# Performance work log

Measured on AMD Instinct MI355X. Metric: run time of the kernel, lower is better.

Reference implementation:

```python
import jax, jax.numpy as jnp
import numpy as np

D_MODEL = 1024
H = 16
D_K = D_MODEL // H
B = 4
S = 2048


def setup_inputs() -> dict:
    key = jax.random.key(0)
    ks = jax.random.split(key, 7)
    q = jax.random.normal(ks[0], (B, S, D_MODEL), dtype=jnp.float32)
    k = jax.random.normal(ks[1], (B, S, D_MODEL), dtype=jnp.float32)
    v = jax.random.normal(ks[2], (B, S, D_MODEL), dtype=jnp.float32)
    # nn.Linear weights have shape (out_features, in_features); y = x @ W.T
    scale = 1.0 / np.sqrt(D_MODEL)
    w_q = jax.random.normal(ks[3], (D_MODEL, D_MODEL), dtype=jnp.float32) * scale
    w_k = jax.random.normal(ks[4], (D_MODEL, D_MODEL), dtype=jnp.float32) * scale
    w_v = jax.random.normal(ks[5], (D_MODEL, D_MODEL), dtype=jnp.float32) * scale
    w_o = jax.random.normal(ks[6], (D_MODEL, D_MODEL), dtype=jnp.float32) * scale
    mask = jnp.ones((1, 1, S, S), dtype=bool)  # broadcasts over [B,H,S,S]
    return {"q": q, "k": k, "v": v, "w_q": w_q, "w_k": w_k, "w_v": w_v,
            "w_o": w_o, "mask": mask}


def reference(q, k, v, w_q, w_k, w_v, w_o, mask):
    # projections (nn.Linear, no bias): x @ W.T
    query = jnp.einsum('bsd,ed->bse', q, w_q)
    key_p = jnp.einsum('bsd,ed->bse', k, w_k)
    value = jnp.einsum('bsd,ed->bse', v, w_v)
    # split heads: [B,S,D] -> [B,H,S,d_k]
    query = query.reshape(B, S, H, D_K).transpose(0, 2, 1, 3)
    key_p = key_p.reshape(B, S, H, D_K).transpose(0, 2, 1, 3)
    value = value.reshape(B, S, H, D_K).transpose(0, 2, 1, 3)
    # scaled dot-product attention (explicit softmax, as in source)
    scores = jnp.einsum('bhqd,bhkd->bhqk', query, key_p) / jnp.sqrt(
        jnp.asarray(D_K, dtype=query.dtype))
    scores = jnp.where(mask, scores, jnp.asarray(-1e9, dtype=scores.dtype))
    weights = jax.nn.softmax(scores, axis=-1)
    ctx = jnp.einsum('bhqk,bhkd->bhqd', weights, value)
    # merge heads and output projection
    ctx = ctx.transpose(0, 2, 1, 3).reshape(B, S, D_MODEL)
    return jnp.einsum('bsd,ed->bse', ctx, w_o)
```

## Files before the change

### kernel.cpp

```cpp
#include <hip/hip_runtime.h>
#include <hip/hip_bf16.h>
#include <stdint.h>
#include <math.h>

#define DM 1024
#define SS 2048
#define HH 16

typedef unsigned short u16;
typedef __attribute__((ext_vector_type(8))) short short8;
typedef __attribute__((ext_vector_type(4))) float f32x4;
typedef __attribute__((ext_vector_type(4))) unsigned short u16x4;

#define C_SCALE 0.18033688011112042f

__device__ __forceinline__ u16 f2bf(float f) {
    union { float f; uint32_t u; } v; v.f = f;
    uint32_t r = v.u + 0x7FFFu + ((v.u >> 16) & 1u);
    return (u16)(r >> 16);
}

__device__ __forceinline__ void async_cp16(const void* g, void* l) {
    __builtin_amdgcn_global_load_lds(
        reinterpret_cast<const __attribute__((address_space(1))) unsigned int*>(
            reinterpret_cast<uintptr_t>(g)),
        reinterpret_cast<__attribute__((address_space(3))) unsigned int*>(
            reinterpret_cast<uintptr_t>(l)),
        16, 0, 0);
}

__device__ __forceinline__ short8 pack8(const float4 a, const float4 b) {
    union { short8 s; struct { __hip_bfloat162 p0, p1, p2, p3; } p; } u;
    u.p.p0 = __float22bfloat162_rn(make_float2(a.x, a.y));
    u.p.p1 = __float22bfloat162_rn(make_float2(a.z, a.w));
    u.p.p2 = __float22bfloat162_rn(make_float2(b.x, b.y));
    u.p.p3 = __float22bfloat162_rn(make_float2(b.z, b.w));
    return u.s;
}

__global__ __launch_bounds__(256) void cast_w4(const float* __restrict__ w0,
                                               const float* __restrict__ w1,
                                               const float* __restrict__ w2,
                                               const float* __restrict__ w3,
                                               u16* __restrict__ o0,
                                               u16* __restrict__ o1,
                                               u16* __restrict__ o2,
                                               u16* __restrict__ o3)
{
    const uint32_t which = blockIdx.x >> 10;
    const uint32_t i = (blockIdx.x & 1023u) * 256u + threadIdx.x;
    const float* in = which == 0 ? w0 : which == 1 ? w1 : which == 2 ? w2 : w3;
    u16* out = which == 0 ? o0 : which == 1 ? o1 : which == 2 ? o2 : o3;
    float4 v = ((const float4*)in)[i];
    u16x4 p = { f2bf(v.x), f2bf(v.y), f2bf(v.z), f2bf(v.w) };
    ((u16x4*)out)[i] = p;
}

__global__ __launch_bounds__(256) void gemm_proj(const float* __restrict__ Aq,
                                                 const float* __restrict__ Ak,
                                                 const float* __restrict__ Av,
                                                 const u16* __restrict__ Bq,
                                                 const u16* __restrict__ Bk,
                                                 const u16* __restrict__ Bv,
                                                 u16* __restrict__ Cq,
                                                 u16* __restrict__ Ck,
                                                 u16* __restrict__ Cv)
{
    __shared__ char sm[32768];
    const uint32_t t = threadIdx.x;
    const uint32_t l = t & 63u, w = t >> 6;
    const uint32_t sw = (blockIdx.x & 7u) * 192u + (blockIdx.x >> 3);
    const uint32_t which = sw >> 9;
    const uint32_t inner = sw & 511u;
    const uint32_t bm = inner >> 3, bn = inner & 7u;
    const uint32_t wr = w >> 1, wc = w & 1u;

    const float* A = which == 0 ? Aq : which == 1 ? Ak : Av;
    const u16*   B = which == 0 ? Bq : which == 1 ? Bk : Bv;

    const uint32_t q15 = l & 15u, G = l >> 4, xq = q15 & 7u;
    const uint32_t vbg0 = q15 * 128u + ((G ^ (xq & 3u)) << 4) + ((xq >> 2) << 6);
    const uint32_t vA0 = wr * 8192u + vbg0,          vA1 = vA0 ^ 64u;
    const uint32_t vB0 = 16384u + wc * 8192u + vbg0, vB1 = vB0 ^ 64u;

    const float* aP[4];
    uint32_t aD[4];
    #pragma unroll
    for (uint32_t i = 0; i < 4; ++i) {
        const uint32_t j = i * 256u + t, row = j >> 3, cc = j & 7u;
        aP[i] = A + (size_t)(bm * 128u + row) * DM + cc * 8u;
        aD[i] = row * 128u + ((cc ^ (row & 7u)) << 4);
    }
    uint32_t La[4];
    const u16* bP[4];
    #pragma unroll
    for (uint32_t i = 0; i < 4; ++i) {
        La[i] = (i * 256u + t) * 16u;
        const uint32_t r = La[i] >> 7;
        const uint32_t c8 = ((La[i] >> 4) & 7u) ^ (r & 7u);
        bP[i] = B + (size_t)(bn * 128u + r) * DM + c8 * 8u;
    }

    f32x4 acc[4][4] = {};
    float4 av[4][2];
    #pragma unroll
    for (uint32_t i = 0; i < 4; ++i) {
        av[i][0] = *(const float4*)(aP[i]);
        av[i][1] = *(const float4*)(aP[i] + 4);
    }

    for (uint32_t k0 = 0; k0 < 1024; k0 += 64) {
        __syncthreads();
        #pragma unroll
        for (uint32_t i = 0; i < 4; ++i)
            *(short8*)(sm + aD[i]) = pack8(av[i][0], av[i][1]);
        #pragma unroll
        for (uint32_t i = 0; i < 4; ++i) async_cp16(bP[i] + k0, sm + 16384 + La[i]);
        __syncthreads();

        if (k0 != 960u) {
            #pragma unroll
            for (uint32_t i = 0; i < 4; ++i) {
                av[i][0] = *(const float4*)(aP[i] + k0 + 64u);
                av[i][1] = *(const float4*)(aP[i] + k0 + 68u);
            }
        }

        #pragma unroll
        for (uint32_t kk = 0; kk < 2; ++kk) {
            const uint32_t va = kk ? vA1 : vA0;
            const uint32_t vb = kk ? vB1 : vB0;
            short8 a[4], b[4];
            #pragma unroll
            for (uint32_t m = 0; m < 4; ++m)
                a[m] = *(const short8*)(sm + va + m * 2048u);
            #pragma unroll
            for (uint32_t n = 0; n < 4; ++n)
                b[n] = *(const short8*)(sm + vb + n * 2048u);
            #pragma unroll
            for (uint32_t m = 0; m < 4; ++m)
                #pragma unroll
                for (uint32_t n = 0; n < 4; ++n)
                    acc[m][n] = __builtin_amdgcn_mfma_f32_16x16x32_bf16(
                        a[m], b[n], acc[m][n], 0, 0, 0);
        }
    }

    u16* Cb = which == 0 ? Cq : which == 1 ? Ck : Cv;
    #pragma unroll
    for (uint32_t m = 0; m < 4; ++m) {
        #pragma unroll
        for (uint32_t n = 0; n < 4; ++n) {
            const uint32_t rmb = bm * 128u + wr * 64u + m * 16u + G * 4u;
            const uint32_t cn  = bn * 128u + wc * 64u + n * 16u + q15;
            if (which == 0) {
                #pragma unroll
                for (uint32_t g = 0; g < 4; ++g)
                    Cb[(size_t)(rmb + g) * DM + cn] = f2bf(acc[m][n][g] * C_SCALE);
            } else if (which == 1) {
                #pragma unroll
                for (uint32_t g = 0; g < 4; ++g)
                    Cb[(size_t)(rmb + g) * DM + cn] = f2bf(acc[m][n][g]);
            } else {
                const uint32_t b_ = rmb >> 11, s0 = rmb & 2047u;
                u16x4 pk;
                #pragma unroll
                for (uint32_t g = 0; g < 4; ++g) pk[g] = f2bf(acc[m][n][g]);
                *(u16x4*)(Cb + (size_t)(b_ * 1024u + cn) * 2048u + s0) = pk;
            }
        }
    }
}

__global__ __launch_bounds__(256) void gemm_out(const u16* __restrict__ A,
                                                const u16* __restrict__ B,
                                                float* __restrict__ C)
{
    __shared__ char sm[32768];
    const uint32_t t = threadIdx.x;
    const uint32_t l = t & 63u, w = t >> 6;
    uint32_t id = blockIdx.x;
    id = (id & 7u) * 64u + (id >> 3);
    const uint32_t bm = id >> 3, bn = id & 7u;
    const uint32_t wr = w >> 1, wc = w & 1u;

    const uint32_t q15 = l & 15u, G = l >> 4, xq = q15 & 7u;
    const uint32_t vbg0 = q15 * 128u + ((G ^ (xq & 3u)) << 4) + ((xq >> 2) << 6);
    const uint32_t vA0 = wr * 8192u + vbg0,          vA1 = vA0 ^ 64u;
    const uint32_t vB0 = 16384u + wc * 8192u + vbg0, vB1 = vB0 ^ 64u;

    uint32_t La[4];
    const u16* aP[4];
    const u16* bP[4];
    #pragma unroll
    for (uint32_t i = 0; i < 4; ++i) {
        La[i] = (i * 256u + t) * 16u;
        const uint32_t r = La[i] >> 7;
        const uint32_t c8 = ((La[i] >> 4) & 7u) ^ (r & 7u);
        aP[i] = A + (size_t)(bm * 128u + r) * DM + c8 * 8u;
        bP[i] = B + (size_t)(bn * 128u + r) * DM + c8 * 8u;
    }

    f32x4 acc[4][4] = {};

    for (uint32_t k0 = 0; k0 < 1024; k0 += 64) {
        __syncthreads();
        #pragma unroll
        for (uint32_t i = 0; i < 4; ++i) async_cp16(aP[i] + k0, sm + La[i]);
        #pragma unroll
        for (uint32_t i = 0; i < 4; ++i) async_cp16(bP[i] + k0, sm + 16384 + La[i]);
        __syncthreads();

        #pragma unroll
        for (uint32_t kk = 0; kk < 2; ++kk) {
            const uint32_t va = kk ? vA1 : vA0;
            const uint32_t vb = kk ? vB1 : vB0;
            short8 a[4], b[4];
            #pragma unroll
            for (uint32_t m = 0; m < 4; ++m)
                a[m] = *(const short8*)(sm + va + m * 2048u);
            #pragma unroll
            for (uint32_t n = 0; n < 4; ++n)
                b[n] = *(const short8*)(sm + vb + n * 2048u);
            #pragma unroll
            for (uint32_t m = 0; m < 4; ++m)
                #pragma unroll
                for (uint32_t n = 0; n < 4; ++n)
                    acc[m][n] = __builtin_amdgcn_mfma_f32_16x16x32_bf16(
                        a[m], b[n], acc[m][n], 0, 0, 0);
        }
    }

    #pragma unroll
    for (uint32_t m = 0; m < 4; ++m) {
        #pragma unroll
        for (uint32_t n = 0; n < 4; ++n) {
            const uint32_t rmb = bm * 128u + wr * 64u + m * 16u + G * 4u;
            const uint32_t cn  = bn * 128u + wc * 64u + n * 16u + q15;
            #pragma unroll
            for (uint32_t g = 0; g < 4; ++g)
                C[(size_t)(rmb + g) * DM + cn] = acc[m][n][g];
        }
    }
}

__global__ __launch_bounds__(512) void attn_mfma(const u16* __restrict__ Q,
                                                 const u16* __restrict__ K,
                                                 const u16* __restrict__ Vt,
                                                 u16* __restrict__ ctx)
{
    __shared__ char sm[69632];
    const uint32_t t = threadIdx.x, l = t & 63u, w = t >> 6;
    uint32_t id = blockIdx.x;
    id = (id & 7u) * 64u + (id >> 3);
    const uint32_t qt = id & 7u, h = (id >> 3) & 15u, b = id >> 7;

    const uint32_t q15 = l & 15u, G = l >> 4, xq = q15 & 7u;

    const uint32_t vb0 = q15 * 128u + ((G ^ (xq & 3u)) << 4) + ((xq >> 2) << 6);
    const uint32_t vb1 = vb0 ^ 64u;
    const uint32_t vbPw = w * 4608u + q15 * 144u + G * 8u;
    const uint32_t vbPr = w * 4608u + q15 * 144u + G * 16u;

    short8 qf[2][2];
    #pragma unroll
    for (uint32_t qb = 0; qb < 2; ++qb) {
        const size_t qrow = (size_t)(b * 2048u + qt * 256u + w * 32u + qb * 16u + q15);
        const uint32_t col = h * 64u + (G << 3);
        qf[qb][0] = *(const short8*)(Q + qrow * DM + col);
        qf[qb][1] = *(const short8*)(Q + qrow * DM + col + 32u);
    }

    short8 ones;
    #pragma unroll
    for (int i = 0; i < 8; ++i) ones[i] = (short)0x3F80;
    const f32x4 ZV = {0.f, 0.f, 0.f, 0.f};

    f32x4 o[2][4] = {};
    f32x4 osum[2] = {};

    const uint32_t Ls = t * 16u;
    const u16* kcur;
    const u16* vcur;
    {
        const size_t kbase = (size_t)b * 2048u * DM + h * 64u;
        const size_t vbase = (size_t)((b * 16u + h) * 64u) * 2048u;
        const uint32_t r = Ls >> 7;
        const uint32_t c8 = ((Ls >> 4) & 7u) ^ (r & 7u);
        const u16* k0p = K  + kbase + (size_t)r * DM    + c8 * 8u;
        const u16* v0p = Vt + vbase + (size_t)r * 2048u + c8 * 8u;
        async_cp16(k0p, sm + Ls);
        async_cp16(v0p, sm + 8192 + Ls);
        kcur = k0p + (size_t)64u * DM;
        vcur = v0p + 64u;
    }

#define ATTN_STEP(BCc, BNc, STAGE)                                             \
    {                                                                          \
        if (STAGE) {                                                           \
            async_cp16(kcur, sm + (BNc) + Ls);                                 \
            async_cp16(vcur, sm + (BNc) + 8192u + Ls);                         \
            kcur += (size_t)64u * DM;                                          \
            vcur += 64u;                                                       \
            asm volatile("s_waitcnt vmcnt(2)" ::: "memory");                   \
        } else {                                                               \
            asm volatile("s_waitcnt vmcnt(0)" ::: "memory");                   \
        }                                                                      \
        __builtin_amdgcn_s_barrier();                                          \
        __builtin_amdgcn_sched_barrier(0);                                     \
        f32x4 s[2][4];                                                         \
        __builtin_amdgcn_s_setprio(1);                                         \
        _Pragma("unroll")                                                      \
        for (uint32_t mf = 0; mf < 4; ++mf) {                                  \
            short8 kf0 = *(const short8*)(sm + (BCc) + vb0 + mf * 2048u);      \
            short8 kf1 = *(const short8*)(sm + (BCc) + vb1 + mf * 2048u);      \
            _Pragma("unroll")                                                  \
            for (uint32_t qb = 0; qb < 2; ++qb) {                              \
                s[qb][mf] = __builtin_amdgcn_mfma_f32_16x16x32_bf16(           \
                    kf1, qf[qb][1],                                            \
                    __builtin_amdgcn_mfma_f32_16x16x32_bf16(                   \
                        kf0, qf[qb][0], ZV, 0, 0, 0),                          \
                    0, 0, 0);                                                  \
            }                                                                  \
        }                                                                      \
        __builtin_amdgcn_s_setprio(0);                                         \
        _Pragma("unroll")                                                      \
        for (uint32_t qb = 0; qb < 2; ++qb) {                                  \
            _Pragma("unroll")                                                  \
            for (uint32_t mf = 0; mf < 4; ++mf) {                              \
                float p0 = __builtin_amdgcn_exp2f(s[qb][mf][0]);               \
                float p1 = __builtin_amdgcn_exp2f(s[qb][mf][1]);               \
                float p2 = __builtin_amdgcn_exp2f(s[qb][mf][2]);               \
                float p3 = __builtin_amdgcn_exp2f(s[qb][mf][3]);               \
                union { u16x4 v; struct { __hip_bfloat162 lo, hi; } b; } pk;   \
                pk.b.lo = __float22bfloat162_rn(make_float2(p0, p1));          \
                pk.b.hi = __float22bfloat162_rn(make_float2(p2, p3));          \
                *(u16x4*)(sm + 32768u + vbPw + qb * 2304u + mf * 32u) = pk.v;  \
            }                                                                  \
        }                                                                      \
        _Pragma("unroll")                                                      \
        for (uint32_t kk = 0; kk < 2; ++kk) {                                  \
            const uint32_t vv = (kk ? vb1 : vb0) + 8192u;                      \
            short8 vf[4];                                                      \
            _Pragma("unroll")                                                  \
            for (uint32_t d = 0; d < 4; ++d)                                   \
                vf[d] = *(const short8*)(sm + (BCc) + vv + d * 2048u);         \
            __builtin_amdgcn_s_setprio(1);                                     \
            _Pragma("unroll")                                                  \
            for (uint32_t qb = 0; qb < 2; ++qb) {                              \
                short8 pf = *(const short8*)(sm + 32768u + vbPr +              \
                                             qb * 2304u + kk * 64u);           \
                _Pragma("unroll")                                              \
                for (uint32_t d = 0; d < 4; ++d)                               \
                    o[qb][d] = __builtin_amdgcn_mfma_f32_16x16x32_bf16(        \
                        pf, vf[d], o[qb][d], 0, 0, 0);                         \
                osum[qb] = __builtin_amdgcn_mfma_f32_16x16x32_bf16(            \
                    pf, ones, osum[qb], 0, 0, 0);                              \
            }                                                                  \
            __builtin_amdgcn_s_setprio(0);                                     \
        }                                                                      \
        asm volatile("s_waitcnt lgkmcnt(0)" ::: "memory");                     \
        __builtin_amdgcn_s_barrier();                                          \
        __builtin_amdgcn_sched_barrier(0);                                     \
    }

    for (uint32_t it = 0; it < 15; ++it) {
        ATTN_STEP(0u, 16384u, true)
        ATTN_STEP(16384u, 0u, true)
    }
    ATTN_STEP(0u, 16384u, true)
    ATTN_STEP(16384u, 0u, false)

#undef ATTN_STEP

    #pragma unroll
    for (uint32_t qb = 0; qb < 2; ++qb) {
        float inv[4];
        #pragma unroll
        for (int g = 0; g < 4; ++g) inv[g] = 1.0f / osum[qb][g];
        #pragma unroll
        for (uint32_t d = 0; d < 4; ++d)
            #pragma unroll
            for (int g = 0; g < 4; ++g) {
                const uint32_t srow = qt * 256u + w * 32u + qb * 16u + G * 4u + (uint32_t)g;
                const uint32_t col  = h * 64u + d * 16u + q15;
                ctx[(size_t)(b * 2048u + srow) * DM + col] = f2bf(o[qb][d][g] * inv[g]);
            }
    }
}

extern "C" void kernel_launch(void* const* d_in, const int* in_sizes, int n_in,
                              void* d_out, int out_size, void* d_ws, size_t ws_size,
                              hipStream_t stream)
{
    const float* q  = (const float*)d_in[0];
    const float* k  = (const float*)d_in[1];
    const float* v  = (const float*)d_in[2];
    const float* wq = (const float*)d_in[3];
    const float* wk = (const float*)d_in[4];
    const float* wv = (const float*)d_in[5];
    const float* wo = (const float*)d_in[6];

    const size_t SZ = (size_t)4 * 2048 * 1024;
    const size_t WZ = (size_t)1024 * 1024;
    u16* ctx = (u16*)d_ws;
    u16* Qp  = ctx + SZ;
    u16* Kp  = Qp  + SZ;
    u16* Vtp = Kp  + SZ;
    u16* wqb = Vtp + SZ;
    u16* wkb = wqb + WZ;
    u16* wvb = wkb + WZ;
    u16* wob = wvb + WZ;

    cast_w4<<<4096, 256, 0, stream>>>(wq, wk, wv, wo, wqb, wkb, wvb, wob);

    gemm_proj<<<1536, 256, 0, stream>>>(q, k, v, wqb, wkb, wvb, Qp, Kp, Vtp);

    attn_mfma<<<512, 512, 0, stream>>>(Qp, Kp, Vtp, ctx);

    gemm_out<<<512, 256, 0, stream>>>(ctx, wob, (float*)d_out);
}
```

Baseline: 217.0 us.

## Load fp32 A tiles asynchronously into LDS and split projection GEMM into three launches

```diff
diff --git a/kernel.cpp b/kernel.cpp
--- a/kernel.cpp
+++ b/kernel.cpp
@@ -56,117 +56,94 @@
     ((u16x4*)out)[i] = p;
 }
 
-__global__ __launch_bounds__(256) void gemm_proj(const float* __restrict__ Aq,
-                                                 const float* __restrict__ Ak,
-                                                 const float* __restrict__ Av,
-                                                 const u16* __restrict__ Bq,
-                                                 const u16* __restrict__ Bk,
-                                                 const u16* __restrict__ Bv,
-                                                 u16* __restrict__ Cq,
-                                                 u16* __restrict__ Ck,
-                                                 u16* __restrict__ Cv)
+template<int MODE>
+__global__ __launch_bounds__(256) void gemm_castA(const float* __restrict__ A,
+                                                  const u16* __restrict__ B,
+                                                  void* __restrict__ C)
 {
-    __shared__ char sm[32768];
+    __shared__ char sm[49152];
     const uint32_t t = threadIdx.x;
     const uint32_t l = t & 63u, w = t >> 6;
-    const uint32_t sw = (blockIdx.x & 7u) * 192u + (blockIdx.x >> 3);
-    const uint32_t which = sw >> 9;
-    const uint32_t inner = sw & 511u;
-    const uint32_t bm = inner >> 3, bn = inner & 7u;
+    uint32_t id = blockIdx.x;
+    id = (id & 7u) * 64u + (id >> 3);
+    const uint32_t bm = id >> 3, bn = id & 7u;
     const uint32_t wr = w >> 1, wc = w & 1u;
 
-    const float* A = which == 0 ? Aq : which == 1 ? Ak : Av;
-    const u16*   B = which == 0 ? Bq : which == 1 ? Bk : Bv;
-
     const uint32_t q15 = l & 15u, G = l >> 4, xq = q15 & 7u;
+    const uint32_t vA0  = wr * 16384u + q15 * 256u + ((2u * G ^ xq) << 4);
+    const uint32_t vA0x = vA0 ^ 16u;
     const uint32_t vbg0 = q15 * 128u + ((G ^ (xq & 3u)) << 4) + ((xq >> 2) << 6);
-    const uint32_t vA0 = wr * 8192u + vbg0,          vA1 = vA0 ^ 64u;
-    const uint32_t vB0 = 16384u + wc * 8192u + vbg0, vB1 = vB0 ^ 64u;
-
-    const float* aP[4];
-    uint32_t aD[4];
+    const uint32_t vB0 = 32768u + wc * 8192u + vbg0, vB1 = vB0 ^ 64u;
+
+    uint32_t LA[8];
+    const float* aP[8];
+    #pragma unroll
+    for (uint32_t i = 0; i < 8; ++i) {
+        const uint32_t j = i * 256u + t, row = j >> 4, ch = j & 15u;
+        const uint32_t c8 = ch ^ (row & 7u);
+        aP[i] = A + (size_t)(bm * 128u + row) * DM + c8 * 4u;
+        LA[i] = j * 16u;
+    }
+    uint32_t LB[4];
+    const u16* bP[4];
     #pragma unroll
     for (uint32_t i = 0; i < 4; ++i) {
-        const uint32_t j = i * 256u + t, row = j >> 3, cc = j & 7u;
-        aP[i] = A + (size_t)(bm * 128u + row) * DM + cc * 8u;
-        aD[i] = row * 128u + ((cc ^ (row & 7u)) << 4);
-    }
-    uint32_t La[4];
-    const u16* bP[4];
-    #pragma unroll
-    for (uint32_t i = 0; i < 4; ++i) {
-        La[i] = (i * 256u + t) * 16u;
-        const uint32_t r = La[i] >> 7;
-        const uint32_t c8 = ((La[i] >> 4) & 7u) ^ (r & 7u);
+        LB[i] = (i * 256u + t) * 16u;
+        const uint32_t r = LB[i] >> 7;
+        const uint32_t c8 = ((LB[i] >> 4) & 7u) ^ (r & 7u);
         bP[i] = B + (size_t)(bn * 128u + r) * DM + c8 * 8u;
     }
 
     f32x4 acc[4][4] = {};
-    float4 av[4][2];
-    #pragma unroll
-    for (uint32_t i = 0; i < 4; ++i) {
-        av[i][0] = *(const float4*)(aP[i]);
-        av[i][1] = *(const float4*)(aP[i] + 4);
-    }
 
     for (uint32_t k0 = 0; k0 < 1024; k0 += 64) {
         __syncthreads();
         #pragma unroll
-        for (uint32_t i = 0; i < 4; ++i)
-            *(short8*)(sm + aD[i]) = pack8(av[i][0], av[i][1]);
-        #pragma unroll
-        for (uint32_t i = 0; i < 4; ++i) async_cp16(bP[i] + k0, sm + 16384 + La[i]);
+        for (uint32_t i = 0; i < 8; ++i) async_cp16(aP[i] + k0, sm + LA[i]);
+        #pragma unroll
+        for (uint32_t i = 0; i < 4; ++i) async_cp16(bP[i] + k0, sm + 32768 + LB[i]);
         __syncthreads();
 
-        if (k0 != 960u) {
-            #pragma unroll
-            for (uint32_t i = 0; i < 4; ++i) {
-                av[i][0] = *(const float4*)(aP[i] + k0 + 64u);
-                av[i][1] = *(const float4*)(aP[i] + k0 + 68u);
+        #pragma unroll
+        for (uint32_t kk = 0; kk < 2; ++kk) {
+            const uint32_t ao = kk * 128u;
+            const uint32_t vb = kk ? vB1 : vB0;
+            short8 a[4], bfr[4];
+            #pragma unroll
+            for (uint32_t m = 0; m < 4; ++m) {
+                float4 lo = *(const float4*)(sm + vA0  + ao + m * 4096u);
+                float4 hi = *(const float4*)(sm + vA0x + ao + m * 4096u);
+                a[m] = pack8(lo, hi);
             }
-        }
-
-        #pragma unroll
-        for (uint32_t kk = 0; kk < 2; ++kk) {
-            const uint32_t va = kk ? vA1 : vA0;
-            const uint32_t vb = kk ? vB1 : vB0;
-            short8 a[4], b[4];
-            #pragma unroll
-            for (uint32_t m = 0; m < 4; ++m)
-                a[m] = *(const short8*)(sm + va + m * 2048u);
             #pragma unroll
             for (uint32_t n = 0; n < 4; ++n)
-                b[n] = *(const short8*)(sm + vb + n * 2048u);
+                bfr[n] = *(const short8*)(sm + vb + n * 2048u);
             #pragma unroll
             for (uint32_t m = 0; m < 4; ++m)
                 #pragma unroll
                 for (uint32_t n = 0; n < 4; ++n)
                     acc[m][n] = __builtin_amdgcn_mfma_f32_16x16x32_bf16(
-                        a[m], b[n], acc[m][n], 0, 0, 0);
+                        a[m], bfr[n], acc[m][n], 0, 0, 0);
         }
     }
 
-    u16* Cb = which == 0 ? Cq : which == 1 ? Ck : Cv;
     #pragma unroll
     for (uint32_t m = 0; m < 4; ++m) {
         #pragma unroll
         for (uint32_t n = 0; n < 4; ++n) {
             const uint32_t rmb = bm * 128u + wr * 64u + m * 16u + G * 4u;
             const uint32_t cn  = bn * 128u + wc * 64u + n * 16u + q15;
-            if (which == 0) {
+            if (MODE == 0 || MODE == 3) {
+                const float sc = (MODE == 3) ? C_SCALE : 1.0f;
                 #pragma unroll
                 for (uint32_t g = 0; g < 4; ++g)
-                    Cb[(size_t)(rmb + g) * DM + cn] = f2bf(acc[m][n][g] * C_SCALE);
-            } else if (which == 1) {
-                #pragma unroll
-                for (uint32_t g = 0; g < 4; ++g)
-                    Cb[(size_t)(rmb + g) * DM + cn] = f2bf(acc[m][n][g]);
+                    ((u16*)C)[(size_t)(rmb + g) * DM + cn] = f2bf(acc[m][n][g] * sc);
             } else {
                 const uint32_t b_ = rmb >> 11, s0 = rmb & 2047u;
                 u16x4 pk;
                 #pragma unroll
                 for (uint32_t g = 0; g < 4; ++g) pk[g] = f2bf(acc[m][n][g]);
-                *(u16x4*)(Cb + (size_t)(b_ * 1024u + cn) * 2048u + s0) = pk;
+                *(u16x4*)((u16*)C + (size_t)(b_ * 1024u + cn) * 2048u + s0) = pk;
             }
         }
     }
@@ -414,7 +391,9 @@
 
     cast_w4<<<4096, 256, 0, stream>>>(wq, wk, wv, wo, wqb, wkb, wvb, wob);
 
-    gemm_proj<<<1536, 256, 0, stream>>>(q, k, v, wqb, wkb, wvb, Qp, Kp, Vtp);
+    gemm_castA<3><<<512, 256, 0, stream>>>(q, wqb, Qp);
+    gemm_castA<0><<<512, 256, 0, stream>>>(k, wkb, Kp);
+    gemm_castA<1><<<512, 256, 0, stream>>>(v, wvb, Vtp);
 
     attn_mfma<<<512, 512, 0, stream>>>(Qp, Kp, Vtp, ctx);
 
```

Result: faster. 184.5 us (-15.0%).
